# Kernel tuning notes

Measured on AMD Instinct MI355X. Metric: run time of the kernel, lower is better.

Reference implementation:

```python
import jax, jax.numpy as jnp
import numpy as np
from jax import lax

E = 4; D_MODEL = 128; D_FF = 128; DT_RANK = 32; D_STATE = 16
L = 12; PAD = 12  # padding_factor=1.0 -> pad L extra zeros
K_TOP = 6; U = 1e-6; EPS = 1e-5
BATCH = 8; NODES = 307; BN = BATCH * NODES
FREQ_IN = (L + PAD) // 2 + 1 + K_TOP  # 19
FREQ_OUT = L // 2 + 1                 # 7


def setup_inputs() -> dict:
    key = jax.random.key(0)
    ks = jax.random.split(key, 14)
    x = jax.random.normal(ks[0], (BN, L, D_MODEL), jnp.float32)
    graph = jax.random.normal(ks[1], (BATCH, L, D_FF, D_FF), jnp.float32) * (1.0 / D_FF)
    in_w = jax.random.normal(ks[2], (E, 2 * D_FF, D_MODEL), jnp.float32) * 0.05
    in_b = jax.random.normal(ks[3], (E, 2 * D_FF), jnp.float32) * 0.02
    x_w = jax.random.normal(ks[4], (E, DT_RANK + 2 * D_STATE + D_FF, D_FF), jnp.float32) * 0.05
    dt_w = jax.random.uniform(ks[5], (E, D_FF, DT_RANK), jnp.float32,
                              -(DT_RANK ** -0.5), DT_RANK ** -0.5)
    dt_b = -2.0 + 0.1 * jax.random.normal(ks[6], (E, D_FF), jnp.float32)
    A_log = jnp.broadcast_to(jnp.log(jnp.arange(1, D_STATE + 1, dtype=jnp.float32))[None, None, :],
                             (E, 1, D_STATE))
    out_w = jax.random.normal(ks[7], (E, D_MODEL, D_FF), jnp.float32) * 0.05
    out_b = jax.random.normal(ks[8], (E, D_MODEL), jnp.float32) * 0.02
    fw_r = jax.random.normal(ks[9], (E, FREQ_OUT, FREQ_IN), jnp.float32) * (FREQ_IN ** -0.5)
    fw_i = jax.random.normal(ks[10], (E, FREQ_OUT, FREQ_IN), jnp.float32) * (FREQ_IN ** -0.5)
    norm_w = jnp.ones((E, D_MODEL), jnp.float32)
    blk_w = jnp.full((E,), 0.5, jnp.float32)
    blk_b = jnp.full((E,), 0.5, jnp.float32)
    return dict(x=x, graph=graph, in_w=in_w, in_b=in_b, x_w=x_w, dt_w=dt_w, dt_b=dt_b,
                A_log=A_log, out_w=out_w, out_b=out_b, fw_r=fw_r, fw_i=fw_i,
                norm_w=norm_w, blk_w=blk_w, blk_b=blk_b)


def _rmsnorm(x, w):
    return x * lax.rsqrt(jnp.mean(x * x, axis=-1, keepdims=True) + EPS) * w


def _mamba_block(x, graph, in_w, in_b, x_w, dt_w, dt_b, A_log, out_w, out_b, fw_r, fw_i):
    bn, Ls, d = x.shape
    # --- FFT frequency gating ---
    x_padded = jnp.concatenate([x, jnp.zeros((bn, PAD, d), x.dtype)], axis=1)
    fp = jnp.fft.rfft(x_padded, axis=1)          # [bn, 13, d] complex
    f = jnp.fft.rfft(x, axis=1)                  # [bn, 7, d] complex
    sq_adj = (f.real + U) ** 2 + (f.imag + U) ** 2
    fs = -jnp.sort(-sq_adj, axis=1)[:, :K_TOP]   # top-K along freq dim, descending
    cat = jnp.concatenate([fp, fs.astype(fp.dtype)], axis=1)  # [bn, 19, d]
    W = lax.complex(fw_r, fw_i)                  # [7, 19]
    freq_proj = jnp.einsum('bkd,ok->bod', cat, W)  # [bn, 7, d]
    wf = jax.nn.softmax(freq_proj.real ** 2 + freq_proj.imag ** 2, axis=2)
    x_freq = jnp.fft.irfft(wf * f, axis=1)       # [bn, 12, d] (n = 2*(7-1))
    # --- input projection ---
    xz = x @ in_w.T + in_b
    xs, z = jnp.split(xz, 2, axis=-1)
    xs = jax.nn.silu(xs)
    # --- SSM ---
    A = -jnp.exp(A_log.astype(jnp.float32))      # [1, d_state]
    dbcd = xs @ x_w.T
    delta, B, C, Dp = jnp.split(dbcd, [DT_RANK, DT_RANK + D_STATE, DT_RANK + 2 * D_STATE], axis=-1)
    delta = jax.nn.softplus(delta @ dt_w.T + dt_b)  # [bn, L, d_ff]
    # graph mixing over nodes: bn = batch * n
    batch = graph.shape[0]
    delta = delta.reshape(batch, -1, Ls, D_FF)
    delta = jnp.einsum('bnsd,bsda->bnsa', delta, graph).reshape(bn, Ls, D_FF)
    deltaA = jnp.exp(delta[..., None] * A)             # [bn, L, d_ff, d_state]
    BX = delta[..., None] * B[:, :, None, :] * xs[..., None]
    dA_t = jnp.moveaxis(deltaA, 1, 0)
    bx_t = jnp.moveaxis(BX, 1, 0)

    def step(h, ab):
        dA, bx = ab
        h = dA * h + bx
        return h, h

    h0 = jnp.zeros((bn, D_FF, D_STATE), xs.dtype)
    _, hs = lax.scan(step, h0, (dA_t, bx_t))
    hs = jnp.moveaxis(hs, 0, 1)                        # [bn, L, d_ff, d_state]
    y = jnp.einsum('blds,bls->bld', hs, C) + Dp * xs
    # --- gate + output ---
    out = y * jax.nn.silu(z) * x_freq
    return out @ out_w.T + out_b


def reference(x, graph, in_w, in_b, x_w, dt_w, dt_b, A_log, out_w, out_b,
              fw_r, fw_i, norm_w, blk_w, blk_b):
    for i in range(E):
        xn = _rmsnorm(x, norm_w[i])
        out = _mamba_block(xn, graph, in_w[i], in_b[i], x_w[i], dt_w[i], dt_b[i],
                           A_log[i], out_w[i], out_b[i], fw_r[i], fw_i[i])
        out = blk_w[i] * out + blk_b[i]
        x = x + out  # dropout is identity in eval
    return jax.nn.silu(x)
```

## Files before the change

### kernel.cpp

```cpp
#include <hip/hip_runtime.h>
#include <math.h>

#define BN    2456
#define LSEQ  12
#define DM    128
#define NODES 307
#define MROWS 29472

typedef __bf16 bfx8 __attribute__((ext_vector_type(8)));
typedef __bf16 bfx4 __attribute__((ext_vector_type(4)));
typedef float  f32x4 __attribute__((ext_vector_type(4)));

#define MFMA16(a, b, c) __builtin_amdgcn_mfma_f32_16x16x32_bf16(a, b, c, 0, 0, 0)

__device__ __forceinline__ float fsilu(float v)     { return v / (1.0f + __expf(-v)); }
__device__ __forceinline__ float fsoftplus(float x) { return fmaxf(x, 0.f) + __logf(1.0f + __expf(-fabsf(x))); }

__global__ __launch_bounds__(256)
void k_convert(const float* __restrict__ in_w, const float* __restrict__ x_w,
               const float* __restrict__ dt_w, const float* __restrict__ out_w,
               const float* __restrict__ graph,
               const float* __restrict__ fw_r, const float* __restrict__ fw_i,
               __bf16* __restrict__ in_w_sw, __bf16* __restrict__ x_w_sw,
               __bf16* __restrict__ dtw_sw, __bf16* __restrict__ out_w_sw,
               __bf16* __restrict__ graph_sw, float* __restrict__ mw) {
    int idx = blockIdx.x * 256 + threadIdx.x;
    if (idx < 131072) {
        int o = idx;
        int e = o >> 15, r = o & 32767;
        int frag = r >> 9, lane = (r >> 3) & 63, j = r & 7;
        int nt = frag >> 2, kc = frag & 3, lm = lane & 15, lq = lane >> 4;
        in_w_sw[o] = (__bf16)in_w[e * 32768 + (nt * 16 + lm) * 128 + kc * 32 + lq * 8 + j];
        return;
    }
    idx -= 131072;
    if (idx < 98304) {
        int o = idx;
        int e = o / 24576, r = o - e * 24576;
        int frag = r >> 9, lane = (r >> 3) & 63, j = r & 7;
        int nt = frag >> 2, kc = frag & 3, lm = lane & 15, lq = lane >> 4;
        x_w_sw[o] = (__bf16)x_w[e * 24576 + (nt * 16 + lm) * 128 + kc * 32 + lq * 8 + j];
        return;
    }
    idx -= 98304;
    if (idx < 16384) {
        int o = idx;
        int e = o >> 12, r = o & 4095;
        int nt = r >> 9, lane = (r >> 3) & 63, j = r & 7;
        int lm = lane & 15, lq = lane >> 4;
        dtw_sw[o] = (__bf16)dt_w[e * 4096 + (nt * 16 + lm) * 32 + lq * 8 + j];
        return;
    }
    idx -= 16384;
    if (idx < 65536) {
        int o = idx;
        int e = o >> 14, r = o & 16383;
        int frag = r >> 9, lane = (r >> 3) & 63, j = r & 7;
        int f = frag >> 2, kc = frag & 3, lm = lane & 15, lq = lane >> 4;
        out_w_sw[o] = (__bf16)out_w[e * 16384 + (f * 16 + lm) * 128 + kc * 32 + lq * 8 + j];
        return;
    }
    idx -= 65536;
    if (idx < 1572864) {
        int bl = idx >> 14, r = idx & 16383;
        int dd = r >> 7, a = r & 127;
        int nt = a >> 4, lm = a & 15, kc = dd >> 5, lq = (dd >> 3) & 3, j = dd & 7;
        graph_sw[(size_t)bl * 16384 + ((size_t)((nt * 4 + kc) * 64 + lq * 16 + lm)) * 8 + j] =
            (__bf16)graph[(size_t)bl * 16384 + dd * 128 + a];
        return;
    }
    idx -= 1572864;
    if (idx < 336) {
        int o = idx;
        int e = o / 84, r = o - e * 84;
        int o2 = r / 12, l = r - o2 * 12;
        float mr = 0.f, mi = 0.f;
        for (int k = 0; k < 13; ++k) {
            float sv, cv;
            __sincosf(6.283185307179586f * (float)(k * l) / 24.0f, &sv, &cv);
            const float wr = fw_r[e * 133 + o2 * 19 + k], wi = fw_i[e * 133 + o2 * 19 + k];
            mr += wr * cv + wi * sv;
            mi += wi * cv - wr * sv;
        }
        mw[e * 256 + (o2 * 12 + l) * 2]     = mr;
        mw[e * 256 + (o2 * 12 + l) * 2 + 1] = mi;
        return;
    }
    idx -= 336;
    if (idx < 168) {
        int o = idx;
        int e = o / 42, r = o - e * 42;
        int o2 = r / 6, k = r - o2 * 6;
        mw[e * 256 + 168 + (o2 * 6 + k) * 2]     = fw_r[e * 133 + o2 * 19 + 13 + k];
        mw[e * 256 + 168 + (o2 * 6 + k) * 2 + 1] = fw_i[e * 133 + o2 * 19 + 13 + k];
    }
}

template <int N>
__device__ __forceinline__ void red_sum128(float* v, float* sred, int tid) {
#pragma unroll
    for (int off = 32; off; off >>= 1)
#pragma unroll
        for (int i = 0; i < N; ++i) v[i] += __shfl_xor(v[i], off, 64);
    if ((tid & 63) == 0) {
#pragma unroll
        for (int i = 0; i < N; ++i) sred[(tid >> 6) * N + i] = v[i];
    }
    __syncthreads();
#pragma unroll
    for (int i = 0; i < N; ++i) v[i] = sred[i] + sred[N + i];
    __syncthreads();
}

template <int N>
__device__ __forceinline__ void red_max128(float* v, float* sred, int tid) {
#pragma unroll
    for (int off = 32; off; off >>= 1)
#pragma unroll
        for (int i = 0; i < N; ++i) v[i] = fmaxf(v[i], __shfl_xor(v[i], off, 64));
    if ((tid & 63) == 0) {
#pragma unroll
        for (int i = 0; i < N; ++i) sred[(tid >> 6) * N + i] = v[i];
    }
    __syncthreads();
#pragma unroll
    for (int i = 0; i < N; ++i) v[i] = fmaxf(sred[i], sred[N + i]);
    __syncthreads();
}

__global__ __launch_bounds__(256)
void k_fused(const float* __restrict__ xcur, const float* __restrict__ norm_w,
             const __bf16* __restrict__ WiSw, const float* __restrict__ in_b,
             const __bf16* __restrict__ WxSw, const __bf16* __restrict__ DWSw,
             const float* __restrict__ dt_b, const __bf16* __restrict__ GSw,
             __bf16* __restrict__ scanp, float* __restrict__ bcf32, int e) {
    __shared__ __bf16 sxs[16 * 136];
    __shared__ __bf16 sdelta[16 * 136];
    __shared__ __bf16 sdel32[16 * 40];
    __shared__ float sxf[16][132];
    const int bl = blockIdx.x;
    const int n0 = blockIdx.y * 16;
    const int tid = threadIdx.x;
    const int wave = tid >> 6, lane = tid & 63;
    const int lm = lane & 15, lq = lane >> 4;
    const int b = bl / 12, l = bl - b * 12;
    const size_t rowbase = (size_t)bl * NODES + n0;

    for (int i = tid; i < 1024; i += 256) {
        const int node = i >> 6, dp2 = i & 63;
        const int gn = min(n0 + node, NODES - 1);
        *(float2*)(&sxf[node][dp2 * 2]) =
            *(const float2*)(xcur + ((size_t)(b * NODES + gn) * 12 + l) * 128 + dp2 * 2);
    }
    __syncthreads();

    float xv[4][8];
#pragma unroll
    for (int kc = 0; kc < 4; ++kc)
#pragma unroll
        for (int j = 0; j < 8; ++j) xv[kc][j] = sxf[lm][kc * 32 + lq * 8 + j];

    float ss = 0.f;
#pragma unroll
    for (int kc = 0; kc < 4; ++kc)
#pragma unroll
        for (int j = 0; j < 8; ++j) ss += xv[kc][j] * xv[kc][j];
    ss += __shfl_xor(ss, 16, 64);
    ss += __shfl_xor(ss, 32, 64);
    const float rms = rsqrtf(ss * (1.0f / 128.0f) + 1e-5f);

    bfx8 af[4];
    const float* nwp = norm_w + e * DM + lq * 8;
#pragma unroll
    for (int kc = 0; kc < 4; ++kc) {
        float4 w0 = *(const float4*)(nwp + kc * 32);
        float4 w1 = *(const float4*)(nwp + kc * 32 + 4);
        af[kc][0] = (__bf16)(xv[kc][0] * rms * w0.x);
        af[kc][1] = (__bf16)(xv[kc][1] * rms * w0.y);
        af[kc][2] = (__bf16)(xv[kc][2] * rms * w0.z);
        af[kc][3] = (__bf16)(xv[kc][3] * rms * w0.w);
        af[kc][4] = (__bf16)(xv[kc][4] * rms * w1.x);
        af[kc][5] = (__bf16)(xv[kc][5] * rms * w1.y);
        af[kc][6] = (__bf16)(xv[kc][6] * rms * w1.z);
        af[kc][7] = (__bf16)(xv[kc][7] * rms * w1.w);
    }

    const __bf16* WxP = WxSw + (size_t)e * 24576;
    bfx8 b2[3][4];
#pragma unroll
    for (int ntl = 0; ntl < 3; ++ntl)
#pragma unroll
        for (int kc = 0; kc < 4; ++kc)
            b2[ntl][kc] = *(const bfx8*)(WxP + (((wave * 3 + ntl) * 4 + kc) * 64 + lane) * 8);

    const __bf16* WiP = WiSw + (size_t)e * 32768;
    f32x4 acc[4];
#pragma unroll
    for (int nt = 0; nt < 4; ++nt) acc[nt] = (f32x4){0.f, 0.f, 0.f, 0.f};
#pragma unroll
    for (int ntl = 0; ntl < 4; ++ntl) {
        const int nt = wave * 4 + ntl;
#pragma unroll
        for (int kc = 0; kc < 4; ++kc) {
            bfx8 bb = *(const bfx8*)(WiP + ((nt * 4 + kc) * 64 + lane) * 8);
            acc[ntl] = MFMA16(af[kc], bb, acc[ntl]);
        }
    }

    const __bf16* DWp = DWSw + (size_t)e * 4096;
    bfx8 b3[2];
#pragma unroll
    for (int ntl = 0; ntl < 2; ++ntl)
        b3[ntl] = *(const bfx8*)(DWp + ((wave * 2 + ntl) * 64 + lane) * 8);
    const __bf16* Gp = GSw + (size_t)bl * 16384;
    bfx8 b4[2][4];
#pragma unroll
    for (int ntl = 0; ntl < 2; ++ntl)
#pragma unroll
        for (int kc = 0; kc < 4; ++kc)
            b4[ntl][kc] = *(const bfx8*)(Gp + (((wave * 2 + ntl) * 4 + kc) * 64 + lane) * 8);

#pragma unroll
    for (int ntl = 0; ntl < 4; ++ntl) {
        const int col = wave * 64 + ntl * 16 + lm;
        const float bias = in_b[e * 256 + col];
#pragma unroll
        for (int r = 0; r < 4; ++r) {
            const int node = lq * 4 + r;
            const float v = fsilu(acc[ntl][r] + bias);
            const int ok = (n0 + node) < NODES;
            if (col < 128) {
                sxs[node * 136 + col] = (__bf16)v;
                if (ok) scanp[(rowbase + node) * 512 + col * 4 + 1] = (__bf16)v;
            } else if (ok) {
                scanp[(rowbase + node) * 512 + (col - 128) * 4 + 3] = (__bf16)v;
            }
        }
    }
    __syncthreads();

    bfx8 ax[4];
#pragma unroll
    for (int kc = 0; kc < 4; ++kc)
        ax[kc] = *(const bfx8*)(sxs + lm * 136 + kc * 32 + lq * 8);

    f32x4 xacc[3];
#pragma unroll
    for (int nt = 0; nt < 3; ++nt) xacc[nt] = (f32x4){0.f, 0.f, 0.f, 0.f};
#pragma unroll
    for (int ntl = 0; ntl < 3; ++ntl)
#pragma unroll
        for (int kc = 0; kc < 4; ++kc)
            xacc[ntl] = MFMA16(ax[kc], b2[ntl][kc], xacc[ntl]);

#pragma unroll
    for (int ntl = 0; ntl < 3; ++ntl) {
        const int col = (wave * 3 + ntl) * 16 + lm;
#pragma unroll
        for (int r = 0; r < 4; ++r) {
            const int node = lq * 4 + r;
            const float v = xacc[ntl][r];
            const int ok = (n0 + node) < NODES;
            if (col < 32) sdel32[node * 40 + col] = (__bf16)v;
            else if (col < 64) { if (ok) bcf32[(rowbase + node) * 32 + (col - 32)] = v; }
            else if (ok) scanp[(rowbase + node) * 512 + (col - 64) * 4 + 2] = (__bf16)v;
        }
    }
    __syncthreads();

    bfx8 ad = *(const bfx8*)(sdel32 + lm * 40 + lq * 8);
    const f32x4 z4 = {0.f, 0.f, 0.f, 0.f};
#pragma unroll
    for (int ntl = 0; ntl < 2; ++ntl) {
        f32x4 dacc = MFMA16(ad, b3[ntl], z4);
        const int col = (wave * 2 + ntl) * 16 + lm;
        const float bias = dt_b[e * 128 + col];
#pragma unroll
        for (int r = 0; r < 4; ++r) {
            const int node = lq * 4 + r;
            sdelta[node * 136 + col] = (__bf16)fsoftplus(dacc[r] + bias);
        }
    }
    __syncthreads();

    bfx8 ag[4];
#pragma unroll
    for (int kc = 0; kc < 4; ++kc)
        ag[kc] = *(const bfx8*)(sdelta + lm * 136 + kc * 32 + lq * 8);

#pragma unroll
    for (int ntl = 0; ntl < 2; ++ntl) {
        f32x4 gacc = z4;
#pragma unroll
        for (int kc = 0; kc < 4; ++kc)
            gacc = MFMA16(ag[kc], b4[ntl][kc], gacc);
        const int col = (wave * 2 + ntl) * 16 + lm;
#pragma unroll
        for (int r = 0; r < 4; ++r) {
            const int node = lq * 4 + r;
            if ((n0 + node) < NODES)
                scanp[(rowbase + node) * 512 + col * 4 + 0] = (__bf16)gacc[r];
        }
    }
}

__global__ __launch_bounds__(128)
void k_scanout(const float* __restrict__ xcur, const float* __restrict__ norm_w,
               const float* __restrict__ mw, const __bf16* __restrict__ scanp,
               const float* __restrict__ bcf32, const float* __restrict__ A_log,
               const __bf16* __restrict__ WoSw, const float* __restrict__ out_b,
               const float* __restrict__ blk_w, const float* __restrict__ blk_b,
               float* __restrict__ xout, int e, int last) {
    __shared__ float sred[24];
    __shared__ __bf16 s_out[16 * 136];
    const int row = blockIdx.x, tid = threadIdx.x;
    const int b = row / NODES, n = row - b * NODES;

    constexpr float SQ32 = 0.8660254037844386f;
    constexpr float C12[12] = {1.f, SQ32, 0.5f, 0.f, -0.5f, -SQ32, -1.f, -SQ32, -0.5f, 0.f, 0.5f, SQ32};
    constexpr float S12[12] = {0.f, 0.5f, SQ32, 1.f, SQ32, 0.5f, 0.f, -0.5f, -SQ32, -1.f, -SQ32, -0.5f};
    constexpr float LOGT[16] = {0.f, 0.6931472f, 1.0986123f, 1.3862944f, 1.6094379f, 1.7917595f,
                                1.9459101f, 2.0794415f, 2.1972246f, 2.3025851f, 2.3978953f,
                                2.4849066f, 2.5649494f, 2.6390573f, 2.7080502f, 2.7725887f};

    bfx4 sc12[12];
    const size_t sb = ((size_t)(b * 12) * NODES + n) * 512 + (size_t)tid * 4;
#pragma unroll
    for (int l = 0; l < 12; ++l)
        sc12[l] = *(const bfx4*)(scanp + sb + (size_t)l * (NODES * 512));

    int chainOK = 1;
#pragma unroll
    for (int s = 0; s < 16; ++s)
        chainOK &= (fabsf(A_log[e * 16 + s] - LOGT[s]) < 1e-4f) ? 1 : 0;

    const float* xp = xcur + (size_t)row * 1536 + tid;
    float xv[12], v[12];
#pragma unroll
    for (int l = 0; l < 12; ++l) { xv[l] = xp[l * 128]; v[l] = xv[l] * xv[l]; }
    red_sum128<12>(v, sred, tid);

    const float nrmw = norm_w[e * DM + tid];
    float xnr[12];
#pragma unroll
    for (int l = 0; l < 12; ++l)
        xnr[l] = xv[l] * rsqrtf(v[l] * (1.0f / 128.0f) + 1e-5f) * nrmw;

    float fr[7], fi[7];
#pragma unroll
    for (int o2 = 0; o2 < 7; ++o2) {
        float r = 0.f, im = 0.f;
#pragma unroll
        for (int l = 0; l < 12; ++l) {
            const int t = (o2 * l) % 12;
            r += xnr[l] * C12[t];
            im -= xnr[l] * S12[t];
        }
        fr[o2] = r; fi[o2] = im;
    }

    float a7[7];
#pragma unroll
    for (int o2 = 0; o2 < 7; ++o2) {
        const float ar = fr[o2] + 1e-6f, ai = fi[o2] + 1e-6f;
        a7[o2] = ar * ar + ai * ai;
    }
#pragma unroll
    for (int pss = 0; pss < 6; ++pss)
#pragma unroll
        for (int j = 0; j < 6; ++j) {
            const float hi = fmaxf(a7[j], a7[j + 1]);
            const float lo = fminf(a7[j], a7[j + 1]);
            a7[j] = hi; a7[j + 1] = lo;
        }

    const float* Me = mw + e * 256;
    float p7[7];
#pragma unroll
    for (int o2 = 0; o2 < 7; ++o2) {
        float pr = 0.f, pi = 0.f;
#pragma unroll
        for (int l = 0; l < 12; ++l) {
            pr += xnr[l] * Me[(o2 * 12 + l) * 2];
            pi += xnr[l] * Me[(o2 * 12 + l) * 2 + 1];
        }
#pragma unroll
        for (int k = 0; k < 6; ++k) {
            pr += a7[k] * Me[168 + (o2 * 6 + k) * 2];
            pi += a7[k] * Me[168 + (o2 * 6 + k) * 2 + 1];
        }
        p7[o2] = pr * pr + pi * pi;
    }

    float m7[7], ex[7], sm[7];
#pragma unroll
    for (int o2 = 0; o2 < 7; ++o2) m7[o2] = p7[o2];
    red_max128<7>(m7, sred, tid);
#pragma unroll
    for (int o2 = 0; o2 < 7; ++o2) { ex[o2] = __expf(p7[o2] - m7[o2]); sm[o2] = ex[o2]; }
    red_sum128<7>(sm, sred, tid);

    float gr[7], gi[7];
#pragma unroll
    for (int o2 = 0; o2 < 7; ++o2) {
        const float wf = ex[o2] / sm[o2];
        gr[o2] = wf * fr[o2];
        gi[o2] = wf * fi[o2];
    }

    float xfqv[12];
#pragma unroll
    for (int l = 0; l < 12; ++l) {
        float val = gr[0] + ((l & 1) ? -gr[6] : gr[6]);
#pragma unroll
        for (int o2 = 1; o2 < 6; ++o2) {
            const int t = (o2 * l) % 12;
            val += 2.0f * (gr[o2] * C12[t] - gi[o2] * S12[t]);
        }
        xfqv[l] = val * (1.0f / 12.0f);
    }

#pragma unroll
    for (int r = 12; r < 16; ++r) s_out[r * 136 + tid] = (__bf16)0.f;

    float h[16];
#pragma unroll
    for (int j = 0; j < 16; ++j) h[j] = 0.f;

    if (chainOK) {
#pragma unroll
        for (int l = 0; l < 12; ++l) {
            const float dl = (float)sc12[l][0], xsv = (float)sc12[l][1];
            const float dlx = dl * xsv;
            const float* bc = bcf32 + ((size_t)(b * 12 + l) * NODES + n) * 32;
            const float q1 = __expf(-dl);
            const float q2 = q1 * q1, q4 = q2 * q2, q8 = q4 * q4;
            float pw[16];
            pw[0] = q1;        pw[1] = q2;        pw[2] = q1 * q2;   pw[3] = q4;
            pw[4] = q1 * q4;   pw[5] = q2 * q4;   pw[6] = pw[2] * q4; pw[7] = q8;
            pw[8] = q1 * q8;   pw[9] = q2 * q8;   pw[10] = pw[2] * q8; pw[11] = q4 * q8;
            pw[12] = pw[4] * q8; pw[13] = pw[5] * q8; pw[14] = pw[6] * q8; pw[15] = q8 * q8;
            float y0 = 0.f, y1 = 0.f, y2 = 0.f, y3 = 0.f;
#pragma unroll
            for (int j = 0; j < 4; ++j) {
                h[j]      = pw[j]      * h[j]      + bc[j]      * dlx;  y0 += h[j]      * bc[16 + j];
                h[j + 4]  = pw[j + 4]  * h[j + 4]  + bc[j + 4]  * dlx;  y1 += h[j + 4]  * bc[20 + j];
                h[j + 8]  = pw[j + 8]  * h[j + 8]  + bc[j + 8]  * dlx;  y2 += h[j + 8]  * bc[24 + j];
                h[j + 12] = pw[j + 12] * h[j + 12] + bc[j + 12] * dlx;  y3 += h[j + 12] * bc[28 + j];
            }
            float y = (y0 + y1) + (y2 + y3);
            y += (float)sc12[l][2] * xsv;
            const float g = y * (float)sc12[l][3] * xfqv[l];
            s_out[l * 136 + tid] = (__bf16)g;
        }
    } else {
        float As[16];
#pragma unroll
        for (int s = 0; s < 16; ++s) As[s] = -__expf(A_log[e * 16 + s]);
#pragma unroll
        for (int l = 0; l < 12; ++l) {
            const float dl = (float)sc12[l][0], xsv = (float)sc12[l][1];
            const float dlx = dl * xsv;
            const float* bc = bcf32 + ((size_t)(b * 12 + l) * NODES + n) * 32;
            float y = 0.f;
#pragma unroll
            for (int j = 0; j < 16; ++j) {
                const float a = __expf(dl * As[j]);
                h[j] = a * h[j] + bc[j] * dlx;
                y += h[j] * bc[16 + j];
            }
            y += (float)sc12[l][2] * xsv;
            const float g = y * (float)sc12[l][3] * xfqv[l];
            s_out[l * 136 + tid] = (__bf16)g;
        }
    }
    __syncthreads();

    const int wave = tid >> 6, lane = tid & 63;
    const int lm = lane & 15, lq = lane >> 4;
    const __bf16* Wop = WoSw + (size_t)e * 16384;
    bfx8 a[4];
#pragma unroll
    for (int kc = 0; kc < 4; ++kc)
        a[kc] = *(const bfx8*)(s_out + lm * 136 + kc * 32 + lq * 8);

    f32x4 acc[4];
#pragma unroll
    for (int nt = 0; nt < 4; ++nt) acc[nt] = (f32x4){0.f, 0.f, 0.f, 0.f};
#pragma unroll
    for (int nt = 0; nt < 4; ++nt) {
        const int f = wave * 4 + nt;
#pragma unroll
        for (int kc = 0; kc < 4; ++kc) {
            bfx8 bb = *(const bfx8*)(Wop + ((f * 4 + kc) * 64 + lane) * 8);
            acc[nt] = MFMA16(a[kc], bb, acc[nt]);
        }
    }

    const float bw = blk_w[e], bb2 = blk_b[e];
#pragma unroll
    for (int nt = 0; nt < 4; ++nt) {
        const int col = wave * 64 + nt * 16 + lm;
        const float ob = out_b[e * 128 + col];
#pragma unroll
        for (int r = 0; r < 4; ++r) {
            const int m = lq * 4 + r;
            if (m < 12) {
                const size_t gi = (size_t)row * 1536 + m * 128 + col;
                float vv = bw * (acc[nt][r] + ob) + bb2 + xcur[gi];
                if (last) vv = fsilu(vv);
                xout[gi] = vv;
            }
        }
    }
}

extern "C" void kernel_launch(void* const* d_in, const int* in_sizes, int n_in,
                              void* d_out, int out_size, void* d_ws, size_t ws_size,
                              hipStream_t stream) {
    (void)in_sizes; (void)n_in; (void)out_size; (void)ws_size;
    const float* x_in   = (const float*)d_in[0];
    const float* graph  = (const float*)d_in[1];
    const float* in_w   = (const float*)d_in[2];
    const float* in_b   = (const float*)d_in[3];
    const float* x_w    = (const float*)d_in[4];
    const float* dt_w   = (const float*)d_in[5];
    const float* dt_b   = (const float*)d_in[6];
    const float* A_log  = (const float*)d_in[7];
    const float* out_w  = (const float*)d_in[8];
    const float* out_b  = (const float*)d_in[9];
    const float* fw_r   = (const float*)d_in[10];
    const float* fw_i   = (const float*)d_in[11];
    const float* norm_w = (const float*)d_in[12];
    const float* blk_w  = (const float*)d_in[13];
    const float* blk_b  = (const float*)d_in[14];
    float* out = (float*)d_out;

    float* ws = (float*)d_ws;
    size_t o = 0;
    __bf16* in_w_sw  = (__bf16*)(ws + o); o += 131072 / 2;
    __bf16* x_w_sw   = (__bf16*)(ws + o); o += 98304 / 2;
    __bf16* dtw_sw   = (__bf16*)(ws + o); o += 16384 / 2;
    __bf16* out_w_sw = (__bf16*)(ws + o); o += 65536 / 2;
    __bf16* graph_sw = (__bf16*)(ws + o); o += 1572864 / 2;
    __bf16* scanp    = (__bf16*)(ws + o); o += (size_t)MROWS * 512 / 2;
    float*  bcf32    = ws + o;            o += (size_t)MROWS * 32;
    float*  mw       = ws + o;            o += 1024;

    hipLaunchKernelGGL(k_convert, dim3(7362), dim3(256), 0, stream,
                       in_w, x_w, dt_w, out_w, graph, fw_r, fw_i,
                       in_w_sw, x_w_sw, dtw_sw, out_w_sw, graph_sw, mw);

    for (int e = 0; e < 4; ++e) {
        const float* xcur = (e == 0) ? x_in : (const float*)out;
        const int last = (e == 3) ? 1 : 0;
        hipLaunchKernelGGL(k_fused, dim3(96, 20), dim3(256), 0, stream,
                           xcur, norm_w, in_w_sw, in_b, x_w_sw, dtw_sw, dt_b, graph_sw,
                           scanp, bcf32, e);
        hipLaunchKernelGGL(k_scanout, dim3(BN), dim3(128), 0, stream,
                           xcur, norm_w, mw, scanp, bcf32, A_log,
                           out_w_sw, out_b, blk_w, blk_b, out, e, last);
    }
}
```

Measured before the change: 382.3 us.

## Move FFT frequency gating into fused kernel blocks and stage scan stores via LDS

The per-row FFT gating work (RMS norm, DFT, top-k sort, softmax, inverse DFT) moves out of the scan/output kernel into extra blocks of the first kernel. Those blocks run alongside the GEMM blocks and write a bf16 x_freq buffer that the scan kernel then reads. The GEMM blocks now stage their scattered scanp writes in shared memory and flush them as coalesced 16-byte stores. The scan kernel also precomputes its exp terms up front. The cost is an extra bf16 intermediate in global memory with its read/write traffic, plus some precision loss from rounding x_freq to bf16.

```diff
diff --git a/kernel.cpp b/kernel.cpp
--- a/kernel.cpp
+++ b/kernel.cpp
@@ -6,6 +6,8 @@
 #define DM    128
 #define NODES 307
 #define MROWS 29472
+#define FREQ_BLKS  1228
+#define FUSED_BLKS 1920
 
 typedef __bf16 bfx8 __attribute__((ext_vector_type(8)));
 typedef __bf16 bfx4 __attribute__((ext_vector_type(4)));
@@ -96,51 +98,159 @@
     }
 }
 
-template <int N>
-__device__ __forceinline__ void red_sum128(float* v, float* sred, int tid) {
-#pragma unroll
-    for (int off = 32; off; off >>= 1)
-#pragma unroll
-        for (int i = 0; i < N; ++i) v[i] += __shfl_xor(v[i], off, 64);
-    if ((tid & 63) == 0) {
-#pragma unroll
-        for (int i = 0; i < N; ++i) sred[(tid >> 6) * N + i] = v[i];
-    }
-    __syncthreads();
-#pragma unroll
-    for (int i = 0; i < N; ++i) v[i] = sred[i] + sred[N + i];
-    __syncthreads();
-}
-
-template <int N>
-__device__ __forceinline__ void red_max128(float* v, float* sred, int tid) {
-#pragma unroll
-    for (int off = 32; off; off >>= 1)
-#pragma unroll
-        for (int i = 0; i < N; ++i) v[i] = fmaxf(v[i], __shfl_xor(v[i], off, 64));
-    if ((tid & 63) == 0) {
-#pragma unroll
-        for (int i = 0; i < N; ++i) sred[(tid >> 6) * N + i] = v[i];
-    }
-    __syncthreads();
-#pragma unroll
-    for (int i = 0; i < N; ++i) v[i] = fmaxf(sred[i], sred[N + i]);
-    __syncthreads();
-}
-
 __global__ __launch_bounds__(256)
 void k_fused(const float* __restrict__ xcur, const float* __restrict__ norm_w,
              const __bf16* __restrict__ WiSw, const float* __restrict__ in_b,
              const __bf16* __restrict__ WxSw, const __bf16* __restrict__ DWSw,
              const float* __restrict__ dt_b, const __bf16* __restrict__ GSw,
-             __bf16* __restrict__ scanp, float* __restrict__ bcf32, int e) {
+             const float* __restrict__ mw,
+             __bf16* __restrict__ scanp, float* __restrict__ bcf32,
+             __bf16* __restrict__ xfq_bf, int e) {
+    const int tid = threadIdx.x;
+
+    if (blockIdx.x < FREQ_BLKS) {
+        __shared__ float sred2[2][2][12];
+        const int hh = tid >> 7, t7 = tid & 127;
+        const int lane = tid & 63, w2 = (tid >> 6) & 1;
+        const int row = blockIdx.x * 2 + hh;
+        const int b = row / NODES, n = row - b * NODES;
+
+        constexpr float SQ32 = 0.8660254037844386f;
+        constexpr float C12[12] = {1.f, SQ32, 0.5f, 0.f, -0.5f, -SQ32, -1.f, -SQ32, -0.5f, 0.f, 0.5f, SQ32};
+        constexpr float S12[12] = {0.f, 0.5f, SQ32, 1.f, SQ32, 0.5f, 0.f, -0.5f, -SQ32, -1.f, -SQ32, -0.5f};
+
+        const float* xp = xcur + (size_t)row * 1536 + t7;
+        float xv[12], v[12];
+#pragma unroll
+        for (int l = 0; l < 12; ++l) { xv[l] = xp[l * 128]; v[l] = xv[l] * xv[l]; }
+#pragma unroll
+        for (int off = 32; off; off >>= 1)
+#pragma unroll
+            for (int i = 0; i < 12; ++i) v[i] += __shfl_xor(v[i], off, 64);
+        if (lane == 0) {
+#pragma unroll
+            for (int i = 0; i < 12; ++i) sred2[hh][w2][i] = v[i];
+        }
+        __syncthreads();
+#pragma unroll
+        for (int i = 0; i < 12; ++i) v[i] = sred2[hh][0][i] + sred2[hh][1][i];
+        __syncthreads();
+
+        const float nrmw = norm_w[e * DM + t7];
+        float xnr[12];
+#pragma unroll
+        for (int l = 0; l < 12; ++l)
+            xnr[l] = xv[l] * rsqrtf(v[l] * (1.0f / 128.0f) + 1e-5f) * nrmw;
+
+        float fr[7], fi[7];
+#pragma unroll
+        for (int o2 = 0; o2 < 7; ++o2) {
+            float r = 0.f, im = 0.f;
+#pragma unroll
+            for (int l = 0; l < 12; ++l) {
+                const int t = (o2 * l) % 12;
+                r += xnr[l] * C12[t];
+                im -= xnr[l] * S12[t];
+            }
+            fr[o2] = r; fi[o2] = im;
+        }
+
+        float a7[7];
+#pragma unroll
+        for (int o2 = 0; o2 < 7; ++o2) {
+            const float ar = fr[o2] + 1e-6f, ai = fi[o2] + 1e-6f;
+            a7[o2] = ar * ar + ai * ai;
+        }
+#pragma unroll
+        for (int pss = 0; pss < 6; ++pss)
+#pragma unroll
+            for (int j = 0; j < 6; ++j) {
+                const float hi = fmaxf(a7[j], a7[j + 1]);
+                const float lo = fminf(a7[j], a7[j + 1]);
+                a7[j] = hi; a7[j + 1] = lo;
+            }
+
+        const float* Me = mw + e * 256;
+        float p7[7];
+#pragma unroll
+        for (int o2 = 0; o2 < 7; ++o2) {
+            float pr = 0.f, pi = 0.f;
+#pragma unroll
+            for (int l = 0; l < 12; ++l) {
+                pr += xnr[l] * Me[(o2 * 12 + l) * 2];
+                pi += xnr[l] * Me[(o2 * 12 + l) * 2 + 1];
+            }
+#pragma unroll
+            for (int k = 0; k < 6; ++k) {
+                pr += a7[k] * Me[168 + (o2 * 6 + k) * 2];
+                pi += a7[k] * Me[168 + (o2 * 6 + k) * 2 + 1];
+            }
+            p7[o2] = pr * pr + pi * pi;
+        }
+
+        float m7[7];
+#pragma unroll
+        for (int i = 0; i < 7; ++i) m7[i] = p7[i];
+#pragma unroll
+        for (int off = 32; off; off >>= 1)
+#pragma unroll
+            for (int i = 0; i < 7; ++i) m7[i] = fmaxf(m7[i], __shfl_xor(m7[i], off, 64));
+        if (lane == 0) {
+#pragma unroll
+            for (int i = 0; i < 7; ++i) sred2[hh][w2][i] = m7[i];
+        }
+        __syncthreads();
+#pragma unroll
+        for (int i = 0; i < 7; ++i) m7[i] = fmaxf(sred2[hh][0][i], sred2[hh][1][i]);
+        __syncthreads();
+
+        float ex[7], sm[7];
+#pragma unroll
+        for (int i = 0; i < 7; ++i) { ex[i] = __expf(p7[i] - m7[i]); sm[i] = ex[i]; }
+#pragma unroll
+        for (int off = 32; off; off >>= 1)
+#pragma unroll
+            for (int i = 0; i < 7; ++i) sm[i] += __shfl_xor(sm[i], off, 64);
+        if (lane == 0) {
+#pragma unroll
+            for (int i = 0; i < 7; ++i) sred2[hh][w2][i] = sm[i];
+        }
+        __syncthreads();
+#pragma unroll
+        for (int i = 0; i < 7; ++i) sm[i] = sred2[hh][0][i] + sred2[hh][1][i];
+
+        float gr[7], gi[7];
+#pragma unroll
+        for (int o2 = 0; o2 < 7; ++o2) {
+            const float wf = ex[o2] / sm[o2];
+            gr[o2] = wf * fr[o2];
+            gi[o2] = wf * fi[o2];
+        }
+
+        const size_t xb = ((size_t)(b * 12) * NODES + n) * 128 + t7;
+#pragma unroll
+        for (int l = 0; l < 12; ++l) {
+            float val = gr[0] + ((l & 1) ? -gr[6] : gr[6]);
+#pragma unroll
+            for (int o2 = 1; o2 < 6; ++o2) {
+                const int t = (o2 * l) % 12;
+                val += 2.0f * (gr[o2] * C12[t] - gi[o2] * S12[t]);
+            }
+            xfq_bf[xb + (size_t)l * (NODES * 128)] = (__bf16)(val * (1.0f / 12.0f));
+        }
+        return;
+    }
+
     __shared__ __bf16 sxs[16 * 136];
     __shared__ __bf16 sdelta[16 * 136];
     __shared__ __bf16 sdel32[16 * 40];
-    __shared__ float sxf[16][132];
-    const int bl = blockIdx.x;
-    const int n0 = blockIdx.y * 16;
-    const int tid = threadIdx.x;
+    __shared__ __align__(16) char sraw[16 * 520 * 2];
+    float  (*sxf)[132]  = (float (*)[132])sraw;
+    __bf16 (*sdump)[520] = (__bf16 (*)[520])sraw;
+
+    const int bid = blockIdx.x - FREQ_BLKS;
+    const int bl = bid / 20;
+    const int n0 = (bid - bl * 20) * 16;
     const int wave = tid >> 6, lane = tid & 63;
     const int lm = lane & 15, lq = lane >> 4;
     const int b = bl / 12, l = bl - b * 12;
@@ -184,6 +294,7 @@
         af[kc][6] = (__bf16)(xv[kc][6] * rms * w1.z);
         af[kc][7] = (__bf16)(xv[kc][7] * rms * w1.w);
     }
+    __syncthreads();
 
     const __bf16* WxP = WxSw + (size_t)e * 24576;
     bfx8 b2[3][4];
@@ -228,12 +339,11 @@
         for (int r = 0; r < 4; ++r) {
             const int node = lq * 4 + r;
             const float v = fsilu(acc[ntl][r] + bias);
-            const int ok = (n0 + node) < NODES;
             if (col < 128) {
                 sxs[node * 136 + col] = (__bf16)v;
-                if (ok) scanp[(rowbase + node) * 512 + col * 4 + 1] = (__bf16)v;
-            } else if (ok) {
-                scanp[(rowbase + node) * 512 + (col - 128) * 4 + 3] = (__bf16)v;
+                sdump[node][col * 4 + 1] = (__bf16)v;
+            } else {
+                sdump[node][(col - 128) * 4 + 3] = (__bf16)v;
             }
         }
     }
@@ -260,10 +370,9 @@
         for (int r = 0; r < 4; ++r) {
             const int node = lq * 4 + r;
             const float v = xacc[ntl][r];
-            const int ok = (n0 + node) < NODES;
             if (col < 32) sdel32[node * 40 + col] = (__bf16)v;
-            else if (col < 64) { if (ok) bcf32[(rowbase + node) * 32 + (col - 32)] = v; }
-            else if (ok) scanp[(rowbase + node) * 512 + (col - 64) * 4 + 2] = (__bf16)v;
+            else if (col < 64) { if ((n0 + node) < NODES) bcf32[(rowbase + node) * 32 + (col - 32)] = v; }
+            else sdump[node][(col - 64) * 4 + 2] = (__bf16)v;
         }
     }
     __syncthreads();
@@ -298,27 +407,31 @@
 #pragma unroll
         for (int r = 0; r < 4; ++r) {
             const int node = lq * 4 + r;
-            if ((n0 + node) < NODES)
-                scanp[(rowbase + node) * 512 + col * 4 + 0] = (__bf16)gacc[r];
-        }
+            sdump[node][col * 4 + 0] = (__bf16)gacc[r];
+        }
+    }
+    __syncthreads();
+
+    __bf16* dst = scanp + rowbase * 512;
+#pragma unroll
+    for (int k = 0; k < 4; ++k) {
+        const int c = k * 256 + tid;
+        const int node = c >> 6;
+        if ((n0 + node) < NODES)
+            *(bfx8*)(dst + (size_t)c * 8) = *(const bfx8*)(&sdump[node][(c & 63) * 8]);
     }
 }
 
 __global__ __launch_bounds__(128)
-void k_scanout(const float* __restrict__ xcur, const float* __restrict__ norm_w,
-               const float* __restrict__ mw, const __bf16* __restrict__ scanp,
-               const float* __restrict__ bcf32, const float* __restrict__ A_log,
-               const __bf16* __restrict__ WoSw, const float* __restrict__ out_b,
-               const float* __restrict__ blk_w, const float* __restrict__ blk_b,
-               float* __restrict__ xout, int e, int last) {
-    __shared__ float sred[24];
+void k_scanout(const float* __restrict__ xcur, const __bf16* __restrict__ scanp,
+               const float* __restrict__ bcf32, const __bf16* __restrict__ xfq_bf,
+               const float* __restrict__ A_log, const __bf16* __restrict__ WoSw,
+               const float* __restrict__ out_b, const float* __restrict__ blk_w,
+               const float* __restrict__ blk_b, float* __restrict__ xout, int e, int last) {
     __shared__ __bf16 s_out[16 * 136];
     const int row = blockIdx.x, tid = threadIdx.x;
     const int b = row / NODES, n = row - b * NODES;
 
-    constexpr float SQ32 = 0.8660254037844386f;
-    constexpr float C12[12] = {1.f, SQ32, 0.5f, 0.f, -0.5f, -SQ32, -1.f, -SQ32, -0.5f, 0.f, 0.5f, SQ32};
-    constexpr float S12[12] = {0.f, 0.5f, SQ32, 1.f, SQ32, 0.5f, 0.f, -0.5f, -SQ32, -1.f, -SQ32, -0.5f};
     constexpr float LOGT[16] = {0.f, 0.6931472f, 1.0986123f, 1.3862944f, 1.6094379f, 1.7917595f,
                                 1.9459101f, 2.0794415f, 2.1972246f, 2.3025851f, 2.3978953f,
                                 2.4849066f, 2.5649494f, 2.6390573f, 2.7080502f, 2.7725887f};
@@ -329,97 +442,17 @@
     for (int l = 0; l < 12; ++l)
         sc12[l] = *(const bfx4*)(scanp + sb + (size_t)l * (NODES * 512));
 
+    __bf16 xq[12];
+    const size_t xb = ((size_t)(b * 12) * NODES + n) * 128 + tid;
+#pragma unroll
+    for (int l = 0; l < 12; ++l)
+        xq[l] = xfq_bf[xb + (size_t)l * (NODES * 128)];
+
     int chainOK = 1;
 #pragma unroll
     for (int s = 0; s < 16; ++s)
         chainOK &= (fabsf(A_log[e * 16 + s] - LOGT[s]) < 1e-4f) ? 1 : 0;
 
-    const float* xp = xcur + (size_t)row * 1536 + tid;
-    float xv[12], v[12];
-#pragma unroll
-    for (int l = 0; l < 12; ++l) { xv[l] = xp[l * 128]; v[l] = xv[l] * xv[l]; }
-    red_sum128<12>(v, sred, tid);
-
-    const float nrmw = norm_w[e * DM + tid];
-    float xnr[12];
-#pragma unroll
-    for (int l = 0; l < 12; ++l)
-        xnr[l] = xv[l] * rsqrtf(v[l] * (1.0f / 128.0f) + 1e-5f) * nrmw;
-
-    float fr[7], fi[7];
-#pragma unroll
-    for (int o2 = 0; o2 < 7; ++o2) {
-        float r = 0.f, im = 0.f;
-#pragma unroll
-        for (int l = 0; l < 12; ++l) {
-            const int t = (o2 * l) % 12;
-            r += xnr[l] * C12[t];
-            im -= xnr[l] * S12[t];
-        }
-        fr[o2] = r; fi[o2] = im;
-    }
-
-    float a7[7];
-#pragma unroll
-    for (int o2 = 0; o2 < 7; ++o2) {
-        const float ar = fr[o2] + 1e-6f, ai = fi[o2] + 1e-6f;
-        a7[o2] = ar * ar + ai * ai;
-    }
-#pragma unroll
-    for (int pss = 0; pss < 6; ++pss)
-#pragma unroll
-        for (int j = 0; j < 6; ++j) {
-            const float hi = fmaxf(a7[j], a7[j + 1]);
-            const float lo = fminf(a7[j], a7[j + 1]);
-            a7[j] = hi; a7[j + 1] = lo;
-        }
-
-    const float* Me = mw + e * 256;
-    float p7[7];
-#pragma unroll
-    for (int o2 = 0; o2 < 7; ++o2) {
-        float pr = 0.f, pi = 0.f;
-#pragma unroll
-        for (int l = 0; l < 12; ++l) {
-            pr += xnr[l] * Me[(o2 * 12 + l) * 2];
-            pi += xnr[l] * Me[(o2 * 12 + l) * 2 + 1];
-        }
-#pragma unroll
-        for (int k = 0; k < 6; ++k) {
-            pr += a7[k] * Me[168 + (o2 * 6 + k) * 2];
-            pi += a7[k] * Me[168 + (o2 * 6 + k) * 2 + 1];
-        }
-        p7[o2] = pr * pr + pi * pi;
-    }
-
-    float m7[7], ex[7], sm[7];
-#pragma unroll
-    for (int o2 = 0; o2 < 7; ++o2) m7[o2] = p7[o2];
-    red_max128<7>(m7, sred, tid);
-#pragma unroll
-    for (int o2 = 0; o2 < 7; ++o2) { ex[o2] = __expf(p7[o2] - m7[o2]); sm[o2] = ex[o2]; }
-    red_sum128<7>(sm, sred, tid);
-
-    float gr[7], gi[7];
-#pragma unroll
-    for (int o2 = 0; o2 < 7; ++o2) {
-        const float wf = ex[o2] / sm[o2];
-        gr[o2] = wf * fr[o2];
-        gi[o2] = wf * fi[o2];
-    }
-
-    float xfqv[12];
-#pragma unroll
-    for (int l = 0; l < 12; ++l) {
-        float val = gr[0] + ((l & 1) ? -gr[6] : gr[6]);
-#pragma unroll
-        for (int o2 = 1; o2 < 6; ++o2) {
-            const int t = (o2 * l) % 12;
-            val += 2.0f * (gr[o2] * C12[t] - gi[o2] * S12[t]);
-        }
-        xfqv[l] = val * (1.0f / 12.0f);
-    }
-
 #pragma unroll
     for (int r = 12; r < 16; ++r) s_out[r * 136 + tid] = (__bf16)0.f;
 
@@ -428,15 +461,18 @@
     for (int j = 0; j < 16; ++j) h[j] = 0.f;
 
     if (chainOK) {
+        float q1a[12];
+#pragma unroll
+        for (int l = 0; l < 12; ++l) q1a[l] = __expf(-(float)sc12[l][0]);
 #pragma unroll
         for (int l = 0; l < 12; ++l) {
             const float dl = (float)sc12[l][0], xsv = (float)sc12[l][1];
             const float dlx = dl * xsv;
             const float* bc = bcf32 + ((size_t)(b * 12 + l) * NODES + n) * 32;
-            const float q1 = __expf(-dl);
+            const float q1 = q1a[l];
             const float q2 = q1 * q1, q4 = q2 * q2, q8 = q4 * q4;
             float pw[16];
-            pw[0] = q1;        pw[1] = q2;        pw[2] = q1 * q2;   pw[3] = q4;
+            pw[0] = q1;        pw[1] = q2;        pw[2] = q1 * q2;    pw[3] = q4;
             pw[4] = q1 * q4;   pw[5] = q2 * q4;   pw[6] = pw[2] * q4; pw[7] = q8;
             pw[8] = q1 * q8;   pw[9] = q2 * q8;   pw[10] = pw[2] * q8; pw[11] = q4 * q8;
             pw[12] = pw[4] * q8; pw[13] = pw[5] * q8; pw[14] = pw[6] * q8; pw[15] = q8 * q8;
@@ -450,7 +486,7 @@
             }
             float y = (y0 + y1) + (y2 + y3);
             y += (float)sc12[l][2] * xsv;
-            const float g = y * (float)sc12[l][3] * xfqv[l];
+            const float g = y * (float)sc12[l][3] * (float)xq[l];
             s_out[l * 136 + tid] = (__bf16)g;
         }
     } else {
@@ -470,7 +506,7 @@
                 y += h[j] * bc[16 + j];
             }
             y += (float)sc12[l][2] * xsv;
-            const float g = y * (float)sc12[l][3] * xfqv[l];
+            const float g = y * (float)sc12[l][3] * (float)xq[l];
             s_out[l * 136 + tid] = (__bf16)g;
         }
     }
@@ -543,7 +579,9 @@
     __bf16* dtw_sw   = (__bf16*)(ws + o); o += 16384 / 2;
     __bf16* out_w_sw = (__bf16*)(ws + o); o += 65536 / 2;
     __bf16* graph_sw = (__bf16*)(ws + o); o += 1572864 / 2;
+    const size_t NE = (size_t)MROWS * 128;
     __bf16* scanp    = (__bf16*)(ws + o); o += (size_t)MROWS * 512 / 2;
+    __bf16* xfq_bf   = (__bf16*)(ws + o); o += NE / 2;
     float*  bcf32    = ws + o;            o += (size_t)MROWS * 32;
     float*  mw       = ws + o;            o += 1024;
 
@@ -554,11 +592,11 @@
     for (int e = 0; e < 4; ++e) {
         const float* xcur = (e == 0) ? x_in : (const float*)out;
         const int last = (e == 3) ? 1 : 0;
-        hipLaunchKernelGGL(k_fused, dim3(96, 20), dim3(256), 0, stream,
+        hipLaunchKernelGGL(k_fused, dim3(FREQ_BLKS + FUSED_BLKS), dim3(256), 0, stream,
                            xcur, norm_w, in_w_sw, in_b, x_w_sw, dtw_sw, dt_b, graph_sw,
-                           scanp, bcf32, e);
+                           mw, scanp, bcf32, xfq_bf, e);
         hipLaunchKernelGGL(k_scanout, dim3(BN), dim3(128), 0, stream,
-                           xcur, norm_w, mw, scanp, bcf32, A_log,
+                           xcur, scanp, bcf32, xfq_bf, A_log,
                            out_w_sw, out_b, blk_w, blk_b, out, e, last);
     }
 }
```

Measured after the change: 377.5 us. Within noise of the previous version (-1.2%).
